# Performance work log

Hardware: AMD Instinct MI355X
Metric: run time of the kernel (lower is better)

## Reference

```python
import jax, jax.numpy as jnp
import numpy as np

N_NODE, K_PATH, L_PATH = 50000, 8, 6
D_NODE, D_PATH = 64, 128
N_EDGE = 1600000


def setup_inputs() -> dict:
    key = jax.random.key(0)
    k1, k2, k3, k4, k5 = jax.random.split(key, 5)
    feat = jax.random.normal(k1, (N_NODE, D_NODE), dtype=jnp.float32)
    weight = jax.random.uniform(k2, (N_EDGE,), dtype=jnp.float32)
    W = jax.random.normal(k3, (D_PATH, D_NODE * (L_PATH - 1)), dtype=jnp.float32) * 0.05
    paths = jax.random.randint(k4, (N_NODE, K_PATH, L_PATH), 0, N_NODE + 1, dtype=jnp.int64)
    edge_ids = jax.random.randint(k5, (N_NODE, K_PATH, L_PATH - 1), 0, N_EDGE, dtype=jnp.int64)
    return {"feat": feat, "weight": weight, "W": W, "paths": paths, "edge_ids": edge_ids}


def reference(feat, weight, W, paths, edge_ids):
    # Pad node features with one zero row: index n_node -> zeros (matches torch cat trick).
    feat_pad = jnp.concatenate([feat, jnp.zeros((1, feat.shape[1]), dtype=feat.dtype)], axis=0)
    # Gather: [n_node, k_path, l_path, d_node]
    path_feat = feat_pad[paths]
    # Edge weights: [n_node, k_path, l_path-1, 1]
    eweight = weight[edge_ids][..., None]
    # Weighted combine of consecutive nodes along the path.
    combined = path_feat[..., : L_PATH - 1, :] + eweight * path_feat[..., 1:L_PATH, :]
    # Flatten last two dims -> [n_node, k_path, d_node*(l_path-1)], then project.
    flat = combined.reshape(combined.shape[0], combined.shape[1], -1)
    return jnp.einsum("nkf,df->nkd", flat, W)
```

## Files before the change

### kernel.cpp

```cpp
#include <hip/hip_runtime.h>
#include <hip/hip_bf16.h>

typedef __bf16 bf16x8 __attribute__((ext_vector_type(8)));
typedef float f32x4 __attribute__((ext_vector_type(4)));

#define N_NODE 50000
#define KPATH 8
#define LPATH 6
#define DNODE 64
#define DPATH 128
#define KDIM 320
#define N_EDGE 1600000
#define NPAIR (N_NODE * KPATH)
#define M_BLK 32
#define NBLK (NPAIR / M_BLK)
#define ROW_BYTES 640
#define WF_BYTES 81920
#define FEATB_BYTES (N_NODE * DNODE * 2)
#define EWB_BYTES (N_EDGE * 2)

#define WF_BLKS   160
#define FEAT_BLKS 1563
#define WGT_BLKS  782
#define PREP_BLKS (WF_BLKS + FEAT_BLKS + WGT_BLKS)

__device__ __forceinline__ int swz(int row, int bytecol) {
    return row * ROW_BYTES + (bytecol ^ ((row & 7) << 4));
}

__global__ void fused_prep(const float* __restrict__ W, __bf16* __restrict__ wf,
                           const float* __restrict__ feat, __bf16* __restrict__ featb,
                           const float* __restrict__ weight, __bf16* __restrict__ ewb) {
    int b = blockIdx.x;
    if (b < WF_BLKS) {
        int t = b * 256 + threadIdx.x;
        if (t >= 8 * 10 * 64 * 8) return;
        int j    = t & 7;
        int lane = (t >> 3) & 63;
        int ks   = (t >> 9) % 10;
        int nt   = t / 5120;
        int k = ks * 32 + (lane >> 4) * 8 + j;
        int n = nt * 16 + (lane & 15);
        wf[t] = (__bf16)W[n * KDIM + k];
    } else if (b < WF_BLKS + FEAT_BLKS) {
        int t = (b - WF_BLKS) * 256 + threadIdx.x;
        if (t >= N_NODE * DNODE / 8) return;
        float4 a = ((const float4*)feat)[t * 2];
        float4 c = ((const float4*)feat)[t * 2 + 1];
        union { bf16x8 v; __bf16 e[8]; } u;
        u.e[0] = (__bf16)a.x; u.e[1] = (__bf16)a.y; u.e[2] = (__bf16)a.z; u.e[3] = (__bf16)a.w;
        u.e[4] = (__bf16)c.x; u.e[5] = (__bf16)c.y; u.e[6] = (__bf16)c.z; u.e[7] = (__bf16)c.w;
        ((bf16x8*)featb)[t] = u.v;
    } else {
        int t = (b - WF_BLKS - FEAT_BLKS) * 256 + threadIdx.x;
        if (t >= N_EDGE / 8) return;
        float4 a = ((const float4*)weight)[t * 2];
        float4 c = ((const float4*)weight)[t * 2 + 1];
        union { bf16x8 v; __bf16 e[8]; } u;
        u.e[0] = (__bf16)a.x; u.e[1] = (__bf16)a.y; u.e[2] = (__bf16)a.z; u.e[3] = (__bf16)a.w;
        u.e[4] = (__bf16)c.x; u.e[5] = (__bf16)c.y; u.e[6] = (__bf16)c.z; u.e[7] = (__bf16)c.w;
        ((bf16x8*)ewb)[t] = u.v;
    }
}

template <int MODE>
__global__ __launch_bounds__(256) void path_gemm(
    const void*  __restrict__ featv,
    const void*  __restrict__ weightv,
    const int*   __restrict__ paths,
    const int*   __restrict__ eids,
    const __bf16* __restrict__ wf,
    float* __restrict__ out)
{
    __shared__ bf16x8 AsVec[M_BLK * ROW_BYTES / 16];
    char* asb = (char*)AsVec;

    const int  t  = threadIdx.x;
    const long p0 = (long)blockIdx.x * M_BLK;
    const int wave = t >> 6;
    const int lane = t & 63;

    bf16x8 breg[10][2];
#pragma unroll
    for (int ks = 0; ks < 10; ++ks)
#pragma unroll
        for (int nt = 0; nt < 2; ++nt)
            breg[ks][nt] = *(const bf16x8*)(wf + (((wave * 2 + nt) * 10 + ks) * 64 + lane) * 8);

    {
        const int  r  = t >> 3;
        const int  s  = t & 7;
        const int  d0 = s * 8;
        const int  lr = r & 7;
        const long p  = p0 + r;

        int pv = 0;
        if (s < LPATH) pv = __builtin_nontemporal_load(paths + p * LPATH + s);
        float wv = 0.f;
        if (s < LPATH - 1) {
            int ev = __builtin_nontemporal_load(eids + p * (LPATH - 1) + s);
            wv = MODE ? (float)((const __bf16*)weightv)[ev]
                      : ((const float*)weightv)[ev];
        }

        int idx[LPATH];
#pragma unroll
        for (int l = 0; l < LPATH; ++l) idx[l] = __shfl(pv, lr * 8 + l, 64);
        float ew[LPATH - 1];
#pragma unroll
        for (int l = 0; l < LPATH - 1; ++l) ew[l] = __shfl(wv, lr * 8 + l, 64);

        float msk[LPATH];
        union { bf16x8 v; __bf16 e[8]; } raw[LPATH];
        float4 rawf[LPATH][2];
#pragma unroll
        for (int l = 0; l < LPATH; ++l) {
            const int id = idx[l];
            msk[l] = (id < N_NODE) ? 1.f : 0.f;
            const long off = (long)(id < N_NODE ? id : 0) * DNODE + d0;
            if (MODE) {
                raw[l].v = *(const bf16x8*)((const __bf16*)featv + off);
            } else {
                const float4* sp = (const float4*)((const float*)featv + off);
                rawf[l][0] = sp[0];
                rawf[l][1] = sp[1];
            }
        }

        float x[8];
#pragma unroll
        for (int i = 0; i < 8; ++i)
            x[i] = MODE ? msk[0] * (float)raw[0].e[i]
                        : msk[0] * ((const float*)&rawf[0][0])[i];
#pragma unroll
        for (int l = 1; l < LPATH; ++l) {
            float y[8];
#pragma unroll
            for (int i = 0; i < 8; ++i)
                y[i] = MODE ? msk[l] * (float)raw[l].e[i]
                            : msk[l] * ((const float*)&rawf[l][0])[i];
            union { bf16x8 v; __bf16 e[8]; } u;
#pragma unroll
            for (int i = 0; i < 8; ++i) u.e[i] = (__bf16)(x[i] + ew[l - 1] * y[i]);
            *(bf16x8*)(asb + swz(r, (l - 1) * 128 + s * 16)) = u.v;
#pragma unroll
            for (int i = 0; i < 8; ++i) x[i] = y[i];
        }
    }
    __syncthreads();

    const int lrow = lane & 15;
    const int h    = lane >> 4;

    f32x4 acc[2][2];
#pragma unroll
    for (int mt = 0; mt < 2; ++mt)
#pragma unroll
        for (int nt = 0; nt < 2; ++nt)
            acc[mt][nt] = (f32x4){0.f, 0.f, 0.f, 0.f};

#pragma unroll
    for (int ks = 0; ks < 10; ++ks) {
#pragma unroll
        for (int mt = 0; mt < 2; ++mt) {
            bf16x8 a = *(const bf16x8*)(asb + swz(mt * 16 + lrow, ks * 64 + h * 16));
            acc[mt][0] = __builtin_amdgcn_mfma_f32_16x16x32_bf16(a, breg[ks][0], acc[mt][0], 0, 0, 0);
            acc[mt][1] = __builtin_amdgcn_mfma_f32_16x16x32_bf16(a, breg[ks][1], acc[mt][1], 0, 0, 0);
        }
    }

    const int rbase = h * 4;
#pragma unroll
    for (int mt = 0; mt < 2; ++mt) {
#pragma unroll
        for (int q = 0; q < 4; ++q) {
            long row = p0 + mt * 16 + rbase + q;
            float* rp = &out[row * DPATH + wave * 32 + lrow];
            __builtin_nontemporal_store(acc[mt][0][q], rp);
            __builtin_nontemporal_store(acc[mt][1][q], rp + 16);
        }
    }
}

extern "C" void kernel_launch(void* const* d_in, const int* in_sizes, int n_in,
                              void* d_out, int out_size, void* d_ws, size_t ws_size,
                              hipStream_t stream) {
    const float* feat   = (const float*)d_in[0];
    const float* weight = (const float*)d_in[1];
    const float* W      = (const float*)d_in[2];
    const int*   paths  = (const int*)d_in[3];
    const int*   eids   = (const int*)d_in[4];
    float* out = (float*)d_out;

    char* ws = (char*)d_ws;
    __bf16* wf    = (__bf16*)ws;
    __bf16* featb = (__bf16*)(ws + WF_BYTES);
    __bf16* ewb   = (__bf16*)(ws + WF_BYTES + FEATB_BYTES);

    if (ws_size >= (size_t)WF_BYTES + FEATB_BYTES + EWB_BYTES) {
        fused_prep<<<PREP_BLKS, 256, 0, stream>>>(W, wf, feat, featb, weight, ewb);
        path_gemm<1><<<NBLK, 256, 0, stream>>>(featb, ewb, paths, eids, wf, out);
    } else {
        fused_prep<<<WF_BLKS, 256, 0, stream>>>(W, wf, feat, featb, weight, ewb);
        path_gemm<0><<<NBLK, 256, 0, stream>>>(feat, weight, paths, eids, wf, out);
    }
}
```

Measured before the change: 119.5 us.

## Pre-gather edge weights in separate kernel and double rows per block

Adds an ew_prep kernel that gathers the bf16 edge weights into a dense per-path array, so the main kernel reads them contiguously instead of doing a random gather. The main kernel's block tile grows from 32 to 64 rows, done as two gather passes, which halves the block count and reuses the register-resident W fragments over more MFMA tiles. It also sets a launch-bounds occupancy hint. The cost is an extra kernel launch, a larger workspace requirement, and more registers and LDS per block.

```diff
diff --git a/kernel.cpp b/kernel.cpp
--- a/kernel.cpp
+++ b/kernel.cpp
@@ -12,12 +12,14 @@
 #define KDIM 320
 #define N_EDGE 1600000
 #define NPAIR (N_NODE * KPATH)
-#define M_BLK 32
+#define NEW (NPAIR * (LPATH - 1))
+#define M_BLK 64
 #define NBLK (NPAIR / M_BLK)
 #define ROW_BYTES 640
 #define WF_BYTES 81920
 #define FEATB_BYTES (N_NODE * DNODE * 2)
 #define EWB_BYTES (N_EDGE * 2)
+#define EWD_BYTES (NEW * 2)
 
 #define WF_BLKS   160
 #define FEAT_BLKS 1563
@@ -63,10 +65,18 @@
     }
 }
 
+__global__ void ew_prep(const __bf16* __restrict__ ewb, const int* __restrict__ eids,
+                        __bf16* __restrict__ ewd, int n) {
+    int t = blockIdx.x * 256 + threadIdx.x;
+    if (t >= n) return;
+    int ev = __builtin_nontemporal_load(eids + t);
+    ewd[t] = ewb[ev];
+}
+
 template <int MODE>
-__global__ __launch_bounds__(256) void path_gemm(
+__global__ __launch_bounds__(256, 4) void path_gemm(
     const void*  __restrict__ featv,
-    const void*  __restrict__ weightv,
+    const void*  __restrict__ wsrc,
     const int*   __restrict__ paths,
     const int*   __restrict__ eids,
     const __bf16* __restrict__ wf,
@@ -88,73 +98,81 @@
             breg[ks][nt] = *(const bf16x8*)(wf + (((wave * 2 + nt) * 10 + ks) * 64 + lane) * 8);
 
     {
-        const int  r  = t >> 3;
         const int  s  = t & 7;
         const int  d0 = s * 8;
-        const int  lr = r & 7;
-        const long p  = p0 + r;
-
-        int pv = 0;
-        if (s < LPATH) pv = __builtin_nontemporal_load(paths + p * LPATH + s);
-        float wv = 0.f;
-        if (s < LPATH - 1) {
-            int ev = __builtin_nontemporal_load(eids + p * (LPATH - 1) + s);
-            wv = MODE ? (float)((const __bf16*)weightv)[ev]
-                      : ((const float*)weightv)[ev];
-        }
-
-        int idx[LPATH];
-#pragma unroll
-        for (int l = 0; l < LPATH; ++l) idx[l] = __shfl(pv, lr * 8 + l, 64);
-        float ew[LPATH - 1];
-#pragma unroll
-        for (int l = 0; l < LPATH - 1; ++l) ew[l] = __shfl(wv, lr * 8 + l, 64);
-
-        float msk[LPATH];
-        union { bf16x8 v; __bf16 e[8]; } raw[LPATH];
-        float4 rawf[LPATH][2];
-#pragma unroll
-        for (int l = 0; l < LPATH; ++l) {
-            const int id = idx[l];
-            msk[l] = (id < N_NODE) ? 1.f : 0.f;
-            const long off = (long)(id < N_NODE ? id : 0) * DNODE + d0;
-            if (MODE) {
-                raw[l].v = *(const bf16x8*)((const __bf16*)featv + off);
-            } else {
-                const float4* sp = (const float4*)((const float*)featv + off);
-                rawf[l][0] = sp[0];
-                rawf[l][1] = sp[1];
+        const int  lr = (t >> 3) & 7;
+
+#pragma unroll
+        for (int pass = 0; pass < 2; ++pass) {
+            const int  r = pass * 32 + (t >> 3);
+            const long p = p0 + r;
+
+            int pv = 0;
+            if (s < LPATH) pv = __builtin_nontemporal_load(paths + p * LPATH + s);
+            float wv = 0.f;
+            if (s < LPATH - 1) {
+                if (MODE) {
+                    wv = (float)__builtin_nontemporal_load(
+                        (const __bf16*)wsrc + p * (LPATH - 1) + s);
+                } else {
+                    int ev = __builtin_nontemporal_load(eids + p * (LPATH - 1) + s);
+                    wv = ((const float*)wsrc)[ev];
+                }
+            }
+
+            int idx[LPATH];
+#pragma unroll
+            for (int l = 0; l < LPATH; ++l) idx[l] = __shfl(pv, lr * 8 + l, 64);
+            float ew[LPATH - 1];
+#pragma unroll
+            for (int l = 0; l < LPATH - 1; ++l) ew[l] = __shfl(wv, lr * 8 + l, 64);
+
+            float msk[LPATH];
+            union { bf16x8 v; __bf16 e[8]; } raw[LPATH];
+            float4 rawf[LPATH][2];
+#pragma unroll
+            for (int l = 0; l < LPATH; ++l) {
+                const int id = idx[l];
+                msk[l] = (id < N_NODE) ? 1.f : 0.f;
+                const long off = (long)(id < N_NODE ? id : 0) * DNODE + d0;
+                if (MODE) {
+                    raw[l].v = *(const bf16x8*)((const __bf16*)featv + off);
+                } else {
+                    const float4* sp = (const float4*)((const float*)featv + off);
+                    rawf[l][0] = sp[0];
+                    rawf[l][1] = sp[1];
+                }
+            }
+
+            float x[8];
+#pragma unroll
+            for (int i = 0; i < 8; ++i)
+                x[i] = MODE ? msk[0] * (float)raw[0].e[i]
+                            : msk[0] * ((const float*)&rawf[0][0])[i];
+#pragma unroll
+            for (int l = 1; l < LPATH; ++l) {
+                float y[8];
+#pragma unroll
+                for (int i = 0; i < 8; ++i)
+                    y[i] = MODE ? msk[l] * (float)raw[l].e[i]
+                                : msk[l] * ((const float*)&rawf[l][0])[i];
+                union { bf16x8 v; __bf16 e[8]; } u;
+#pragma unroll
+                for (int i = 0; i < 8; ++i) u.e[i] = (__bf16)(x[i] + ew[l - 1] * y[i]);
+                *(bf16x8*)(asb + swz(r, (l - 1) * 128 + s * 16)) = u.v;
+#pragma unroll
+                for (int i = 0; i < 8; ++i) x[i] = y[i];
             }
         }
-
-        float x[8];
-#pragma unroll
-        for (int i = 0; i < 8; ++i)
-            x[i] = MODE ? msk[0] * (float)raw[0].e[i]
-                        : msk[0] * ((const float*)&rawf[0][0])[i];
-#pragma unroll
-        for (int l = 1; l < LPATH; ++l) {
-            float y[8];
-#pragma unroll
-            for (int i = 0; i < 8; ++i)
-                y[i] = MODE ? msk[l] * (float)raw[l].e[i]
-                            : msk[l] * ((const float*)&rawf[l][0])[i];
-            union { bf16x8 v; __bf16 e[8]; } u;
-#pragma unroll
-            for (int i = 0; i < 8; ++i) u.e[i] = (__bf16)(x[i] + ew[l - 1] * y[i]);
-            *(bf16x8*)(asb + swz(r, (l - 1) * 128 + s * 16)) = u.v;
-#pragma unroll
-            for (int i = 0; i < 8; ++i) x[i] = y[i];
-        }
     }
     __syncthreads();
 
     const int lrow = lane & 15;
     const int h    = lane >> 4;
 
-    f32x4 acc[2][2];
-#pragma unroll
-    for (int mt = 0; mt < 2; ++mt)
+    f32x4 acc[4][2];
+#pragma unroll
+    for (int mt = 0; mt < 4; ++mt)
 #pragma unroll
         for (int nt = 0; nt < 2; ++nt)
             acc[mt][nt] = (f32x4){0.f, 0.f, 0.f, 0.f};
@@ -162,7 +180,7 @@
 #pragma unroll
     for (int ks = 0; ks < 10; ++ks) {
 #pragma unroll
-        for (int mt = 0; mt < 2; ++mt) {
+        for (int mt = 0; mt < 4; ++mt) {
             bf16x8 a = *(const bf16x8*)(asb + swz(mt * 16 + lrow, ks * 64 + h * 16));
             acc[mt][0] = __builtin_amdgcn_mfma_f32_16x16x32_bf16(a, breg[ks][0], acc[mt][0], 0, 0, 0);
             acc[mt][1] = __builtin_amdgcn_mfma_f32_16x16x32_bf16(a, breg[ks][1], acc[mt][1], 0, 0, 0);
@@ -171,7 +189,7 @@
 
     const int rbase = h * 4;
 #pragma unroll
-    for (int mt = 0; mt < 2; ++mt) {
+    for (int mt = 0; mt < 4; ++mt) {
 #pragma unroll
         for (int q = 0; q < 4; ++q) {
             long row = p0 + mt * 16 + rbase + q;
@@ -196,10 +214,12 @@
     __bf16* wf    = (__bf16*)ws;
     __bf16* featb = (__bf16*)(ws + WF_BYTES);
     __bf16* ewb   = (__bf16*)(ws + WF_BYTES + FEATB_BYTES);
-
-    if (ws_size >= (size_t)WF_BYTES + FEATB_BYTES + EWB_BYTES) {
+    __bf16* ewd   = (__bf16*)(ws + WF_BYTES + FEATB_BYTES + EWB_BYTES);
+
+    if (ws_size >= (size_t)WF_BYTES + FEATB_BYTES + EWB_BYTES + EWD_BYTES) {
         fused_prep<<<PREP_BLKS, 256, 0, stream>>>(W, wf, feat, featb, weight, ewb);
-        path_gemm<1><<<NBLK, 256, 0, stream>>>(featb, ewb, paths, eids, wf, out);
+        ew_prep<<<(NEW + 255) / 256, 256, 0, stream>>>(ewb, eids, ewd, NEW);
+        path_gemm<1><<<NBLK, 256, 0, stream>>>(featb, ewd, paths, eids, wf, out);
     } else {
         fused_prep<<<WF_BLKS, 256, 0, stream>>>(W, wf, feat, featb, weight, ewb);
         path_gemm<0><<<NBLK, 256, 0, stream>>>(feat, weight, paths, eids, wf, out);
```

Result: slower. 146.5 us (+22.5%).
